# Kernel tuning notes

Measured on AMD Instinct MI355X. Metric: run time of the kernel, lower is better.

## Reference

```python
import jax, jax.numpy as jnp
import numpy as np

N_LAYERS = 12
N_CH = 256
N_IN = 4
KS = 3
SPECT_CH = 640


def conv1d(x, w, b, dilation):
    # x: [B, T, Cin], w: [K, Cin, Cout] (WIO), SAME padding, given dilation
    y = jax.lax.conv_general_dilated(
        x, w, window_strides=(1,), padding='SAME',
        rhs_dilation=(dilation,), dimension_numbers=('NWC', 'WIO', 'NWC'))
    return y + b


def setup_inputs() -> dict:
    key = jax.random.key(0)
    ks = jax.random.split(key, 16)
    s = 0.02
    inp = {}
    inp['audio'] = jax.random.normal(ks[0], (8, 4096, N_IN), dtype=jnp.float32)
    inp['spect'] = jax.random.normal(ks[1], (8, 4096, SPECT_CH), dtype=jnp.float32)
    # start 1x1 conv: [Cin, Cout]
    inp['w_start'] = jax.random.normal(ks[2], (N_IN, N_CH), dtype=jnp.float32) * s
    inp['b_start'] = jnp.zeros((N_CH,), dtype=jnp.float32)
    # dilated in_layers: stacked [L, K, Cin, 2*Cout]
    inp['w_in'] = jax.random.normal(ks[3], (N_LAYERS, KS, N_CH, 2 * N_CH), dtype=jnp.float32) * s
    inp['b_in'] = jnp.zeros((N_LAYERS, 2 * N_CH), dtype=jnp.float32)
    # cond 1x1 convs: stacked [L, SPECT_CH, 2*Cout]
    inp['w_cond'] = jax.random.normal(ks[4], (N_LAYERS, SPECT_CH, 2 * N_CH), dtype=jnp.float32) * s
    inp['b_cond'] = jnp.zeros((N_LAYERS, 2 * N_CH), dtype=jnp.float32)
    # res_skip 1x1 convs: first L-1 have 2*Cout, last has Cout
    inp['w_res'] = jax.random.normal(ks[5], (N_LAYERS - 1, N_CH, 2 * N_CH), dtype=jnp.float32) * s
    inp['b_res'] = jnp.zeros((N_LAYERS - 1, 2 * N_CH), dtype=jnp.float32)
    inp['w_res_last'] = jax.random.normal(ks[6], (N_CH, N_CH), dtype=jnp.float32) * s
    inp['b_res_last'] = jnp.zeros((N_CH,), dtype=jnp.float32)
    # end 1x1 conv (zero-initialized in the original; use small random for a
    # non-degenerate numerical baseline)
    inp['w_end'] = jax.random.normal(ks[7], (N_CH, 2 * N_IN), dtype=jnp.float32) * s
    inp['b_end'] = jnp.zeros((2 * N_IN,), dtype=jnp.float32)
    return inp


def reference(audio, spect, w_start, b_start, w_in, b_in, w_cond, b_cond,
              w_res, b_res, w_res_last, b_res_last, w_end, b_end):
    # start: 1x1 conv == matmul over channels
    started = jnp.einsum('btc,cd->btd', audio, w_start) + b_start  # [B,T,256]
    # precompute all conditioning projections: [L,B,T,512]
    cond_all = jnp.einsum('btc,lcd->lbtd', spect, w_cond) + b_cond[:, None, None, :]
    output = None
    for i in range(N_LAYERS):
        in_l = conv1d(started, w_in[i], b_in[i], 2 ** i)  # [B,T,512]
        acts = in_l + cond_all[i]
        half_tanh = jnp.tanh(acts[..., :N_CH])
        half_sig = jax.nn.sigmoid(acts[..., N_CH:])
        activated = half_tanh * half_sig  # [B,T,256]
        if i < N_LAYERS - 1:
            rs = jnp.einsum('btc,cd->btd', activated, w_res[i]) + b_res[i]
            started = started + rs[..., :N_CH]
            skip = rs[..., N_CH:]
        else:
            skip = jnp.einsum('btc,cd->btd', activated, w_res_last) + b_res_last
        output = skip if output is None else output + skip
    out = jnp.einsum('btc,cd->btd', output, w_end) + b_end  # [B,T,2*N_IN]
    return out
```

## Files before the change

kernel.cpp:

```cpp
#include <hip/hip_runtime.h>
#include <cstdint>

#define PAD 2048
#define KG 1408

typedef float f32x4 __attribute__((ext_vector_type(4)));
typedef __bf16 bf16x8 __attribute__((ext_vector_type(8)));
typedef __bf16 bf16x4 __attribute__((ext_vector_type(4)));

__device__ __forceinline__ void g2l16(const void* g, void* l) {
    __builtin_amdgcn_global_load_lds(
        (__attribute__((address_space(1))) void*)(uintptr_t)g,
        (__attribute__((address_space(3))) void*)(uint32_t)(uintptr_t)l,
        16, 0, 0);
}


__global__ void cvt_bf16_kernel(const float4* __restrict__ src, bf16x4* __restrict__ dst, int n4) {
    int idx = blockIdx.x * 256 + threadIdx.x;
    if (idx < n4) {
        float4 v = src[idx];
        bf16x4 o = {(__bf16)v.x, (__bf16)v.y, (__bf16)v.z, (__bf16)v.w};
        dst[idx] = o;
    }
}

__global__ void init_started_kernel(const float* __restrict__ audio, const float* __restrict__ w_start,
                                    const float* __restrict__ b_start, __bf16* __restrict__ started_pad) {
    int pr = blockIdx.x * 4 + (threadIdx.x >> 6);
    int c0 = (threadIdx.x & 63) * 4;
    int off = pr & 8191;
    bf16x4 o = {(__bf16)0.f, (__bf16)0.f, (__bf16)0.f, (__bf16)0.f};
    if (off >= PAD && off < PAD + 4096) {
        int r = ((pr >> 13) << 12) + (off - PAD);
        float a0 = audio[r * 4 + 0], a1 = audio[r * 4 + 1], a2 = audio[r * 4 + 2], a3 = audio[r * 4 + 3];
        for (int j = 0; j < 4; ++j) {
            int c = c0 + j;
            o[j] = (__bf16)(b_start[c] + a0 * w_start[c] + a1 * w_start[256 + c]
                            + a2 * w_start[512 + c] + a3 * w_start[768 + c]);
        }
    }
    *(bf16x4*)&started_pad[(size_t)pr * 256 + c0] = o;
}

__global__ void transpose_gate(const float* __restrict__ w_in, const float* __restrict__ w_cond,
                               __bf16* __restrict__ Wg) {
    __shared__ float tile[64][65];
    int i = blockIdx.z;
    int k0 = blockIdx.y * 64, n0 = blockIdx.x * 64;
    int tid = threadIdx.x, c = tid & 63, rr = tid >> 6;
    for (int it = 0; it < 16; ++it) {
        int kl = it * 4 + rr;
        int k = k0 + kl;
        int np = n0 + c;
        int phys = ((np >> 4) & 1) * 256 + (np >> 5) * 16 + (np & 15);
        float v;
        if (k < 768) v = w_in[((i * 3 + (k >> 8)) * 256 + (k & 255)) * 512 + phys];
        else         v = w_cond[(i * 640 + (k - 768)) * 512 + phys];
        tile[kl][c] = v;
    }
    __syncthreads();
    for (int it = 0; it < 16; ++it) {
        int nl = it * 4 + rr;
        Wg[(size_t)(i * 512 + n0 + nl) * KG + k0 + c] = (__bf16)tile[c][nl];
    }
}

__global__ void transpose_kn(const float* __restrict__ src, __bf16* __restrict__ dst,
                             int K, int N, int srcLS, int dstLS) {
    __shared__ float tile[64][65];
    int i = blockIdx.z;
    int k0 = blockIdx.y * 64, n0 = blockIdx.x * 64;
    int tid = threadIdx.x, c = tid & 63, rr = tid >> 6;
    const float* s = src + (size_t)i * srcLS;
    __bf16* dp = dst + (size_t)i * dstLS;
    for (int it = 0; it < 16; ++it) {
        int kl = it * 4 + rr;
        tile[kl][c] = s[(k0 + kl) * N + n0 + c];
    }
    __syncthreads();
    for (int it = 0; it < 16; ++it) {
        int nl = it * 4 + rr;
        dp[(size_t)(n0 + nl) * K + k0 + c] = (__bf16)tile[c][nl];
    }
}

__global__ void bias_gate_kernel(const float* __restrict__ b_in, const float* __restrict__ b_cond,
                                 float* __restrict__ bias) {
    int idx = blockIdx.x * 256 + threadIdx.x;
    int i = idx >> 9, np = idx & 511;
    int phys = ((np >> 4) & 1) * 256 + (np >> 5) * 16 + (np & 15);
    bias[idx] = b_in[i * 512 + phys] + b_cond[i * 512 + phys];
}

__global__ void wfold_kernel(const float* __restrict__ w_res, const float* __restrict__ w_res_last,
                             const float* __restrict__ w_end, const float* __restrict__ b_res,
                             const float* __restrict__ b_res_last, const float* __restrict__ b_end,
                             float* __restrict__ wfold, float* __restrict__ outconst) {
    if (blockIdx.x == 96) {
        __shared__ float red[256][8];
        int j = threadIdx.x;
        float bsum = b_res_last[j];
        for (int i = 0; i < 11; ++i) bsum += b_res[i * 512 + 256 + j];
        for (int c = 0; c < 8; ++c) red[j][c] = bsum * w_end[j * 8 + c];
        __syncthreads();
        if (j < 8) {
            float s = b_end[j];
            for (int t = 0; t < 256; ++t) s += red[t][j];
            outconst[j] = s;
        }
        return;
    }
    int idx = blockIdx.x * 256 + threadIdx.x;
    int i = idx >> 11, rem = idx & 2047, k = rem >> 3, c = rem & 7;
    float s = 0.f;
    if (i < 11) {
        const float* wr = w_res + (size_t)(i * 256 + k) * 512 + 256;
        for (int j = 0; j < 256; ++j) s += wr[j] * w_end[j * 8 + c];
    } else {
        const float* wr = w_res_last + k * 256;
        for (int j = 0; j < 256; ++j) s += wr[j] * w_end[j * 8 + c];
    }
    wfold[idx] = s;
}


__global__ __launch_bounds__(512, 2) void gate_kernel(
    const __bf16* __restrict__ started_pad, const __bf16* __restrict__ spect,
    const __bf16* __restrict__ Wg,
    const float* __restrict__ bias,
    __bf16* __restrict__ activated, int d) {
    __shared__ __align__(16) __bf16 SMEM[65536];
    const int tid = threadIdx.x;
    const int m0 = blockIdx.x * 256;
    const int n0 = blockIdx.y * 256;
    const int padbase = ((m0 >> 12) << 13) + PAD + (m0 & 4095);
    const int wave = tid >> 6, lane = tid & 63;
    const int wr = wave >> 2, wc = wave & 3;
    const int quad = lane >> 4, l15 = lane & 15;

    const int srow = tid >> 2;
    const int scw = ((tid & 3) * 8) ^ (((tid >> 3) & 3) << 3);

    f32x4 acc[8][4];
    #pragma unroll
    for (int i = 0; i < 8; i++)
        #pragma unroll
        for (int j = 0; j < 4; j++) acc[i][j] = f32x4{0.f, 0.f, 0.f, 0.f};

    auto stageA = [&](int kt, int s) {
        const __bf16* g0;
        int rs;
        if (kt < 24) {
            int tap = kt >> 3;
            int cb = (kt & 7) * 32;
            g0 = started_pad + (padbase + (tap - 1) * d) * 256 + cb + scw;
            rs = 256;
        } else {
            int cb = (kt - 24) * 32;
            g0 = spect + (size_t)m0 * 640 + cb + scw;
            rs = 640;
        }
        __bf16* As = SMEM + s * 8192;
        g2l16(g0 + srow * rs, As + tid * 8);
        g2l16(g0 + (128 + srow) * rs, As + 4096 + tid * 8);
    };
    auto stageB = [&](int kt, int s) {
        const __bf16* g0 = Wg + (size_t)(n0 + srow) * KG + kt * 32 + scw;
        __bf16* Bs = SMEM + 32768 + s * 8192;
        g2l16(g0, Bs + tid * 8);
        g2l16(g0 + 128 * KG, Bs + 4096 + tid * 8);
    };

    stageA(0, 0); stageB(0, 0);
    stageA(1, 1); stageB(1, 1);
    asm volatile("s_waitcnt vmcnt(4)" ::: "memory");
    __builtin_amdgcn_s_barrier();

    for (int j = 0; j < 44; ++j) {
        const int s = j & 3;
        const __bf16* Asl = SMEM + s * 8192;
        const __bf16* Bsl = SMEM + 32768 + s * 8192;

        bf16x8 b[4];
        #pragma unroll
        for (int nf = 0; nf < 4; ++nf) {
            int br = wc * 64 + nf * 16 + l15;
            b[nf] = *(const bf16x8*)&Bsl[br * 32 + ((quad * 8) ^ (((br >> 1) & 3) << 3))];
        }
        bf16x8 a[4];
        #pragma unroll
        for (int f = 0; f < 4; ++f) {
            int ar = wr * 128 + f * 16 + l15;
            a[f] = *(const bf16x8*)&Asl[ar * 32 + ((quad * 8) ^ (((ar >> 1) & 3) << 3))];
        }
        if (j + 2 < 44) stageA(j + 2, (j + 2) & 3);
        __builtin_amdgcn_s_barrier();
        __builtin_amdgcn_s_setprio(1);
        #pragma unroll
        for (int f = 0; f < 4; ++f)
            #pragma unroll
            for (int nf = 0; nf < 4; ++nf)
                acc[f][nf] = __builtin_amdgcn_mfma_f32_16x16x32_bf16(a[f], b[nf], acc[f][nf], 0, 0, 0);
        __builtin_amdgcn_s_setprio(0);
        __builtin_amdgcn_s_barrier();
        #pragma unroll
        for (int f = 0; f < 4; ++f) {
            int ar = wr * 128 + 64 + f * 16 + l15;
            a[f] = *(const bf16x8*)&Asl[ar * 32 + ((quad * 8) ^ (((ar >> 1) & 3) << 3))];
        }
        if (j + 2 < 44) stageB(j + 2, (j + 2) & 3);
        if (j + 1 < 44) {
            if (j + 2 < 44) asm volatile("s_waitcnt vmcnt(4)" ::: "memory");
            else            asm volatile("s_waitcnt vmcnt(0)" ::: "memory");
        }
        __builtin_amdgcn_s_barrier();
        __builtin_amdgcn_s_setprio(1);
        #pragma unroll
        for (int f = 0; f < 4; ++f)
            #pragma unroll
            for (int nf = 0; nf < 4; ++nf)
                acc[4 + f][nf] = __builtin_amdgcn_mfma_f32_16x16x32_bf16(a[f], b[nf], acc[4 + f][nf], 0, 0, 0);
        __builtin_amdgcn_s_setprio(0);
        __builtin_amdgcn_s_barrier();
    }

    __bf16* tile = SMEM;
    #pragma unroll
    for (int nj = 0; nj < 2; ++nj) {
        int colT = wc * 64 + nj * 32 + l15;
        float bt = bias[n0 + colT];
        float bs = bias[n0 + colT + 16];
        int chl = wc * 32 + nj * 16 + l15;
        #pragma unroll
        for (int mi = 0; mi < 8; ++mi) {
            #pragma unroll
            for (int reg = 0; reg < 4; ++reg) {
                int row = wr * 128 + mi * 16 + quad * 4 + reg;
                float xt = acc[mi][2 * nj][reg] + bt;
                float xs = acc[mi][2 * nj + 1][reg] + bs;
                float th = 2.f / (1.f + __expf(-2.f * xt)) - 1.f;
                float sg = 1.f / (1.f + __expf(-xs));
                tile[row * 132 + chl] = (__bf16)(th * sg);
            }
        }
    }
    __syncthreads();
    int chb = n0 >> 1;
    for (int pass = 0; pass < 8; ++pass) {
        int row = (tid >> 4) + 32 * pass;
        int seg = tid & 15;
        bf16x8 v = *(const bf16x8*)&tile[row * 132 + seg * 8];
        *(bf16x8*)&activated[(m0 + row) * 256 + chb + seg * 8] = v;
    }
}

__global__ __launch_bounds__(256) void res_kernel(
    const __bf16* __restrict__ activated, const __bf16* __restrict__ Wr,
    const float* __restrict__ b_res,
    const float* __restrict__ wfold,
    const float* __restrict__ outconst,
    __bf16* __restrict__ started_pad, float* __restrict__ out, int initOut) {
    __shared__ __align__(16) __bf16 As[128 * 32];
    __shared__ __align__(16) __bf16 Bs[128 * 32];
    __shared__ __align__(16) __bf16 WfB[16 * 264];
    const int tid = threadIdx.x;
    const int m0 = blockIdx.x * 128;
    const int n0 = blockIdx.y * 128;
    const int srow = tid >> 2;
    const int skq = (tid & 3) * 8;
    const int wave = tid >> 6, lane = tid & 63;
    const int wm = (wave >> 1) * 64, wn = (wave & 1) * 64;
    const int quad = lane >> 4, l15 = lane & 15;
    const bool doOut = (blockIdx.y == 0);
    const bool outWave = doOut && (wn == 0);

    f32x4 acc[4][4];
    for (int i = 0; i < 4; i++)
        for (int j = 0; j < 4; j++) acc[i][j] = f32x4{0.f, 0.f, 0.f, 0.f};
    f32x4 acc_o[4];
    for (int i = 0; i < 4; i++) acc_o[i] = f32x4{0.f, 0.f, 0.f, 0.f};

    const __bf16* Abase = activated + (m0 + srow) * 256 + skq;
    const __bf16* Bbase = Wr + (n0 + srow) * 256 + skq;

    if (doOut) {
        for (int t = 0; t < 16; ++t) {
            int e = t * 256 + tid;
            int col = e >> 8, k = e & 255;
            WfB[col * 264 + k] = (col < 8) ? (__bf16)wfold[k * 8 + col] : (__bf16)0.f;
        }
    }

    for (int ks = 0; ks < 8; ++ks) {
        int kk = ks * 32;
        g2l16(Abase + kk, &As[srow * 32 + skq]);
        g2l16(Abase + kk + 64 * 256, &As[(64 + srow) * 32 + skq]);
        g2l16(Bbase + kk, &Bs[srow * 32 + skq]);
        g2l16(Bbase + kk + 64 * 256, &Bs[(64 + srow) * 32 + skq]);
        __syncthreads();
        bf16x8 a[4], b[4];
        for (int mi = 0; mi < 4; mi++) a[mi] = *(const bf16x8*)&As[(wm + mi * 16 + l15) * 32 + quad * 8];
        for (int ni = 0; ni < 4; ni++) b[ni] = *(const bf16x8*)&Bs[(wn + ni * 16 + l15) * 32 + quad * 8];
        for (int mi = 0; mi < 4; mi++)
            for (int ni = 0; ni < 4; ni++)
                acc[mi][ni] = __builtin_amdgcn_mfma_f32_16x16x32_bf16(a[mi], b[ni], acc[mi][ni], 0, 0, 0);
        if (outWave) {
            bf16x8 bx = *(const bf16x8*)&WfB[l15 * 264 + kk + quad * 8];
            for (int mi = 0; mi < 4; mi++)
                acc_o[mi] = __builtin_amdgcn_mfma_f32_16x16x32_bf16(a[mi], bx, acc_o[mi], 0, 0, 0);
        }
        __syncthreads();
    }

    for (int ni = 0; ni < 4; ++ni) {
        int col = n0 + wn + ni * 16 + l15;
        float bcol = b_res[col];
        for (int mi = 0; mi < 4; ++mi) {
            for (int reg = 0; reg < 4; ++reg) {
                int r = m0 + wm + mi * 16 + quad * 4 + reg;
                int pr = ((r >> 12) << 13) + PAD + (r & 4095);
                int idx = pr * 256 + col;
                float f = (float)started_pad[idx] + acc[mi][ni][reg] + bcol;
                started_pad[idx] = (__bf16)f;
            }
        }
    }
    if (outWave && l15 < 8) {
        for (int mi = 0; mi < 4; ++mi) {
            for (int reg = 0; reg < 4; ++reg) {
                int r = m0 + wm + mi * 16 + quad * 4 + reg;
                float base = initOut ? outconst[l15] : out[r * 8 + l15];
                out[r * 8 + l15] = base + acc_o[mi][reg];
            }
        }
    }
}

__global__ __launch_bounds__(256) void outacc_kernel(
    const __bf16* __restrict__ activated, const float* __restrict__ wfold,
    float* __restrict__ out) {
    __shared__ __align__(16) float Wf[2048];
    int tid = threadIdx.x;
    ((float4*)Wf)[tid] = ((const float4*)wfold)[tid];
    ((float4*)Wf)[256 + tid] = ((const float4*)wfold)[256 + tid];
    __syncthreads();
    int row2 = tid >> 1, half = tid & 1;
    int r = blockIdx.x * 128 + row2;
    const bf16x8* ap = (const bf16x8*)(activated + r * 256);
    const float4* wf = (const float4*)Wf;
    float ox = 0.f, oy = 0.f, oz = 0.f, ow = 0.f;
    for (int c8 = 0; c8 < 32; ++c8) {
        bf16x8 av = ap[c8];
        for (int e = 0; e < 8; ++e) {
            float a = (float)av[e];
            float4 w = wf[(c8 * 8 + e) * 2 + half];
            ox += a * w.x; oy += a * w.y; oz += a * w.z; ow += a * w.w;
        }
    }
    float4* op = (float4*)&out[r * 8 + half * 4];
    float4 o = *op;
    o.x += ox; o.y += oy; o.z += oz; o.w += ow;
    *op = o;
}


extern "C" void kernel_launch(void* const* d_in, const int* in_sizes, int n_in,
                              void* d_out, int out_size, void* d_ws, size_t ws_size,
                              hipStream_t stream) {
    const float* audio      = (const float*)d_in[0];
    const float* spect      = (const float*)d_in[1];
    const float* w_start    = (const float*)d_in[2];
    const float* b_start    = (const float*)d_in[3];
    const float* w_in       = (const float*)d_in[4];
    const float* b_in       = (const float*)d_in[5];
    const float* w_cond     = (const float*)d_in[6];
    const float* b_cond     = (const float*)d_in[7];
    const float* w_res      = (const float*)d_in[8];
    const float* b_res      = (const float*)d_in[9];
    const float* w_res_last = (const float*)d_in[10];
    const float* b_res_last = (const float*)d_in[11];
    const float* w_end      = (const float*)d_in[12];
    const float* b_end      = (const float*)d_in[13];
    float* out = (float*)d_out;

    char* ws = (char*)d_ws;
    __bf16* started_pad = (__bf16*)ws; ws += 33554432;
    __bf16* activated   = (__bf16*)ws; ws += 16777216;
    __bf16* spect_bf    = (__bf16*)ws; ws += 41943040;
    __bf16* Wg          = (__bf16*)ws; ws += 17301504;
    __bf16* Wr          = (__bf16*)ws; ws += 1441792;
    float*  wfold       = (float*)ws;  ws += 98304;
    float*  biasg       = (float*)ws;  ws += 24576;
    float*  outconst    = (float*)ws;  ws += 256;

    init_started_kernel<<<dim3(16384), 256, 0, stream>>>(audio, w_start, b_start, started_pad);
    cvt_bf16_kernel<<<dim3(20480), 256, 0, stream>>>((const float4*)spect, (bf16x4*)spect_bf, 5242880);
    transpose_gate<<<dim3(8, 22, 12), 256, 0, stream>>>(w_in, w_cond, Wg);
    transpose_kn<<<dim3(4, 4, 11), 256, 0, stream>>>(w_res, Wr, 256, 512, 256 * 512, 256 * 256);
    bias_gate_kernel<<<dim3(24), 256, 0, stream>>>(b_in, b_cond, biasg);
    wfold_kernel<<<dim3(97), 256, 0, stream>>>(w_res, w_res_last, w_end, b_res, b_res_last, b_end,
                                               wfold, outconst);

    for (int i = 0; i < 12; ++i) {
        gate_kernel<<<dim3(128, 2), 512, 0, stream>>>(
            started_pad, spect_bf, Wg + (size_t)i * 512 * KG, biasg + i * 512, activated, 1 << i);
        if (i < 11) {
            res_kernel<<<dim3(256, 2), 256, 0, stream>>>(
                activated, Wr + (size_t)i * 256 * 256, b_res + i * 512,
                wfold + i * 2048, outconst, started_pad, out, i == 0 ? 1 : 0);
        } else {
            outacc_kernel<<<dim3(256), 256, 0, stream>>>(activated, wfold + 11 * 2048, out);
        }
    }
}
```

Before: 1.056 ms.

## Double-buffer LDS fragments in registers and cut per-iteration barriers to one

Restructures the bf16 MFMA main loop so the A and B fragments for the next k-step are read from LDS into registers while the current step's MFMAs run. The four s_barriers per iteration become a single barrier, and the vmcnt waits are retuned to match the new issue order. The aim is to hide LDS read latency and cut barrier stalls between waves. In exchange it holds extra fragment registers (b_nxt, a_nxt), which could raise register pressure, lower occupancy, or cause spills.

```diff
diff --git a/kernel.cpp b/kernel.cpp
--- a/kernel.cpp
+++ b/kernel.cpp
@@ -175,55 +175,76 @@
     stageA(0, 0); stageB(0, 0);
     stageA(1, 1); stageB(1, 1);
     asm volatile("s_waitcnt vmcnt(4)" ::: "memory");
-    __builtin_amdgcn_s_barrier();
+    asm volatile("s_barrier" ::: "memory");
+
+    bf16x8 a_cur[4], b_cur[4], b_nxt[4];
+    {
+        const __bf16* Asl = SMEM;
+        const __bf16* Bsl = SMEM + 32768;
+        #pragma unroll
+        for (int f = 0; f < 4; ++f) {
+            int ar = wr * 128 + f * 16 + l15;
+            a_cur[f] = *(const bf16x8*)&Asl[ar * 32 + ((quad * 8) ^ (((ar >> 1) & 3) << 3))];
+        }
+        #pragma unroll
+        for (int nf = 0; nf < 4; ++nf) {
+            int br = wc * 64 + nf * 16 + l15;
+            b_cur[nf] = *(const bf16x8*)&Bsl[br * 32 + ((quad * 8) ^ (((br >> 1) & 3) << 3))];
+        }
+    }
 
     for (int j = 0; j < 44; ++j) {
         const int s = j & 3;
+        const int sn = (j + 1) & 3;
         const __bf16* Asl = SMEM + s * 8192;
-        const __bf16* Bsl = SMEM + 32768 + s * 8192;
-
-        bf16x8 b[4];
-        #pragma unroll
-        for (int nf = 0; nf < 4; ++nf) {
-            int br = wc * 64 + nf * 16 + l15;
-            b[nf] = *(const bf16x8*)&Bsl[br * 32 + ((quad * 8) ^ (((br >> 1) & 3) << 3))];
-        }
-        bf16x8 a[4];
-        #pragma unroll
-        for (int f = 0; f < 4; ++f) {
-            int ar = wr * 128 + f * 16 + l15;
-            a[f] = *(const bf16x8*)&Asl[ar * 32 + ((quad * 8) ^ (((ar >> 1) & 3) << 3))];
-        }
+
         if (j + 2 < 44) stageA(j + 2, (j + 2) & 3);
-        __builtin_amdgcn_s_barrier();
-        __builtin_amdgcn_s_setprio(1);
-        #pragma unroll
-        for (int f = 0; f < 4; ++f)
-            #pragma unroll
-            for (int nf = 0; nf < 4; ++nf)
-                acc[f][nf] = __builtin_amdgcn_mfma_f32_16x16x32_bf16(a[f], b[nf], acc[f][nf], 0, 0, 0);
-        __builtin_amdgcn_s_setprio(0);
-        __builtin_amdgcn_s_barrier();
+        bf16x8 a_nxt[4];
         #pragma unroll
         for (int f = 0; f < 4; ++f) {
             int ar = wr * 128 + 64 + f * 16 + l15;
-            a[f] = *(const bf16x8*)&Asl[ar * 32 + ((quad * 8) ^ (((ar >> 1) & 3) << 3))];
-        }
+            a_nxt[f] = *(const bf16x8*)&Asl[ar * 32 + ((quad * 8) ^ (((ar >> 1) & 3) << 3))];
+        }
+        if (j + 2 < 44) asm volatile("s_waitcnt vmcnt(2)" ::: "memory");
+        else            asm volatile("s_waitcnt vmcnt(0)" ::: "memory");
+        __builtin_amdgcn_s_setprio(1);
+        #pragma unroll
+        for (int f = 0; f < 4; ++f)
+            #pragma unroll
+            for (int nf = 0; nf < 4; ++nf)
+                acc[f][nf] = __builtin_amdgcn_mfma_f32_16x16x32_bf16(a_cur[f], b_cur[nf], acc[f][nf], 0, 0, 0);
+        __builtin_amdgcn_s_setprio(0);
+        asm volatile("s_barrier" ::: "memory");
+
         if (j + 2 < 44) stageB(j + 2, (j + 2) & 3);
         if (j + 1 < 44) {
-            if (j + 2 < 44) asm volatile("s_waitcnt vmcnt(4)" ::: "memory");
-            else            asm volatile("s_waitcnt vmcnt(0)" ::: "memory");
-        }
-        __builtin_amdgcn_s_barrier();
+            const __bf16* Anl = SMEM + sn * 8192;
+            const __bf16* Bnl = SMEM + 32768 + sn * 8192;
+            #pragma unroll
+            for (int f = 0; f < 4; ++f) {
+                int ar = wr * 128 + f * 16 + l15;
+                a_cur[f] = *(const bf16x8*)&Anl[ar * 32 + ((quad * 8) ^ (((ar >> 1) & 3) << 3))];
+            }
+            #pragma unroll
+            for (int nf = 0; nf < 4; ++nf) {
+                int br = wc * 64 + nf * 16 + l15;
+                b_nxt[nf] = *(const bf16x8*)&Bnl[br * 32 + ((quad * 8) ^ (((br >> 1) & 3) << 3))];
+            }
+        }
         __builtin_amdgcn_s_setprio(1);
         #pragma unroll
         for (int f = 0; f < 4; ++f)
             #pragma unroll
             for (int nf = 0; nf < 4; ++nf)
-                acc[4 + f][nf] = __builtin_amdgcn_mfma_f32_16x16x32_bf16(a[f], b[nf], acc[4 + f][nf], 0, 0, 0);
+                acc[4 + f][nf] = __builtin_amdgcn_mfma_f32_16x16x32_bf16(a_nxt[f], b_cur[nf], acc[4 + f][nf], 0, 0, 0);
         __builtin_amdgcn_s_setprio(0);
-        __builtin_amdgcn_s_barrier();
-    }
+        if (j + 1 < 44) {
+            #pragma unroll
+            for (int nf = 0; nf < 4; ++nf) b_cur[nf] = b_nxt[nf];
+        }
+    }
+
+    __syncthreads();
 
     __bf16* tile = SMEM;
     #pragma unroll
```

New measurement: 1.036 ms. No clear change (-1.9%).
